# Optimization experiments

Measured on AMD Instinct MI355X. Metric: run time of the kernel, lower is better.

## Reference

```python
import jax, jax.numpy as jnp
import numpy as np

D_MODEL = 1024
NUM_HEADS = 16
HEAD_DIM = D_MODEL // NUM_HEADS


def setup_inputs() -> dict:
    key = jax.random.key(0)
    ks = jax.random.split(key, 11)
    B, S = 2, 2048
    scale = 1.0 / np.sqrt(D_MODEL)
    inp = {
        "query": jax.random.normal(ks[0], (B, S, D_MODEL), jnp.float32),
        "key": jax.random.normal(ks[1], (B, S, D_MODEL), jnp.float32),
        "value": jax.random.normal(ks[2], (B, S, D_MODEL), jnp.float32),
        "Wq": jax.random.normal(ks[3], (D_MODEL, D_MODEL), jnp.float32) * scale,
        "bq": jnp.zeros((D_MODEL,), jnp.float32),
        "Wk": jax.random.normal(ks[4], (D_MODEL, D_MODEL), jnp.float32) * scale,
        "bk": jnp.zeros((D_MODEL,), jnp.float32),
        "Wv": jax.random.normal(ks[5], (D_MODEL, D_MODEL), jnp.float32) * scale,
        "bv": jnp.zeros((D_MODEL,), jnp.float32),
        "Wo": jax.random.normal(ks[6], (D_MODEL, D_MODEL), jnp.float32) * scale,
        "bo": jnp.zeros((D_MODEL,), jnp.float32),
    }
    return inp


def _split_heads(x):
    # [B, S, D] -> [B, H, S, Dh]
    B, S, _ = x.shape
    return x.reshape(B, S, NUM_HEADS, HEAD_DIM).transpose(0, 2, 1, 3)


def reference(query, key, value, Wq, bq, Wk, bk, Wv, bv, Wo, bo):
    q = _split_heads(query @ Wq.T + bq)   # [B,H,S,Dh]
    k = _split_heads(key @ Wk.T + bk)
    v = _split_heads(value @ Wv.T + bv)
    scores = jnp.einsum('bhqd,bhkd->bhqk', q, k) / jnp.sqrt(
        jnp.asarray(HEAD_DIM, q.dtype))
    probs = jax.nn.softmax(scores, axis=-1)
    ctx = jnp.einsum('bhqk,bhkd->bhqd', probs, v)  # [B,H,S,Dh]
    B, H, S, Dh = ctx.shape
    ctx = ctx.transpose(0, 2, 1, 3).reshape(B, S, H * Dh)  # [B,S,D]
    return ctx @ Wo.T + bo
```

## Files before the change

### kernel.cpp

```cpp
#include <hip/hip_runtime.h>
#include <hip/hip_bf16.h>
#include <stdint.h>

#define D_MODEL 1024
#define NHEADS  16
#define HDIM    64
#define BATCH   2
#define SEQ     2048
#define MROWS   (BATCH*SEQ)

typedef __attribute__((ext_vector_type(8))) short  bf16x8;
typedef __attribute__((ext_vector_type(4))) float  f32x4;
typedef __attribute__((ext_vector_type(4))) int    int4v;

__device__ __forceinline__ unsigned short f2bf(float f) {
  unsigned int u = __float_as_uint(f);
  u = (u + 0x7fffu + ((u >> 16) & 1u)) >> 16;
  return (unsigned short)u;
}

__device__ __forceinline__ unsigned cvtpk_bf16(float lo, float hi) {
  unsigned r;
  asm("v_cvt_pk_bf16_f32 %0, %1, %2" : "=v"(r) : "v"(lo), "v"(hi));
  return r;
}

__device__ __forceinline__ int4v pack8(const float4& x, const float4& y) {
  int4v r;
  r[0] = (int)cvtpk_bf16(x.x, x.y);
  r[1] = (int)cvtpk_bf16(x.z, x.w);
  r[2] = (int)cvtpk_bf16(y.x, y.y);
  r[3] = (int)cvtpk_bf16(y.z, y.w);
  return r;
}

__device__ __forceinline__ void gload_lds16(const unsigned short* g, unsigned short* l) {
  __builtin_amdgcn_global_load_lds(
      (const __attribute__((address_space(1))) void*)g,
      (__attribute__((address_space(3))) void*)l,
      16, 0, 0);
}

__device__ __forceinline__ int swz_chunk(int row) { return (row + (row >> 3)) & 7; }
__device__ __forceinline__ int swz4(int row) { return (row + (row >> 2)) & 3; }
__device__ __forceinline__ int kperm(int m) {
  return (m & 0x63) | ((m & 0x10) >> 2) | ((m & 0x0C) << 1);
}

struct CvtArgs {
  const float* src[6];
  unsigned short* dst[6];
  int n[6];
};

__global__ __launch_bounds__(256) void cvt_all(CvtArgs a) {
  int t = blockIdx.y;
  const float* s = a.src[t];
  unsigned short* d = a.dst[t];
  int n = a.n[t];
  int stride = gridDim.x * blockDim.x * 4;
  for (int i = (blockIdx.x * blockDim.x + threadIdx.x) * 4; i < n; i += stride) {
    float4 v = *(const float4*)(s + i);
    ushort4 o;
    o.x = f2bf(v.x); o.y = f2bf(v.y); o.z = f2bf(v.z); o.w = f2bf(v.w);
    *(ushort4*)(d + i) = o;
  }
}

__device__ __forceinline__ void gemm_core(const unsigned short* __restrict__ X,
                                          const unsigned short* __restrict__ W,
                                          int m0, int n0,
                                          unsigned short* As, unsigned short* Bs,
                                          f32x4 (&acc)[4][4]) {
  const int tid  = threadIdx.x;
  const int lane = tid & 63;
  const int wv   = tid >> 6;
  const int wr   = wv >> 1, wc = wv & 1;
  const int srow = tid >> 3;
  const int scol = (((tid & 7) ^ (srow & 7)) * 8);
  const int sdst = tid * 16;

  for (int kt = 0; kt < D_MODEL / 64; ++kt) {
    __syncthreads();
    const unsigned short* Xs = X + (size_t)m0 * D_MODEL + kt * 64;
    const unsigned short* Ws = W + (size_t)n0 * D_MODEL + kt * 64;
#pragma unroll
    for (int c = 0; c < 4; ++c) {
      gload_lds16(Xs + (size_t)(srow + c * 32) * D_MODEL + scol,
                  (unsigned short*)((char*)As + sdst + c * 4096));
      gload_lds16(Ws + (size_t)(srow + c * 32) * D_MODEL + scol,
                  (unsigned short*)((char*)Bs + sdst + c * 4096));
    }
    __syncthreads();
#pragma unroll
    for (int kc = 0; kc < 2; ++kc) {
      bf16x8 af[4], bfv[4];
#pragma unroll
      for (int i = 0; i < 4; ++i) {
        int arow  = wr * 64 + i * 16 + (lane & 15);
        int abyte = (arow * 128 + (kc * 32 + 8 * (lane >> 4)) * 2) ^ ((arow & 7) << 4);
        af[i] = *(const bf16x8*)((const char*)As + abyte);
        int brow  = wc * 64 + i * 16 + (lane & 15);
        int bbyte = (brow * 128 + (kc * 32 + 8 * (lane >> 4)) * 2) ^ ((brow & 7) << 4);
        bfv[i] = *(const bf16x8*)((const char*)Bs + bbyte);
      }
#pragma unroll
      for (int mi = 0; mi < 4; ++mi)
#pragma unroll
        for (int ni = 0; ni < 4; ++ni)
          acc[mi][ni] = __builtin_amdgcn_mfma_f32_16x16x32_bf16(af[mi], bfv[ni],
                                                                acc[mi][ni], 0, 0, 0);
    }
  }
}

__global__ __launch_bounds__(256) void gemm_qkv(
    const unsigned short* __restrict__ Xq, const unsigned short* __restrict__ Xk,
    const unsigned short* __restrict__ Xv,
    const unsigned short* __restrict__ Wq, const unsigned short* __restrict__ Wk,
    const unsigned short* __restrict__ Wv,
    const float* __restrict__ bq, const float* __restrict__ bk,
    const float* __restrict__ bv,
    unsigned short* __restrict__ oq, unsigned short* __restrict__ ok,
    unsigned short* __restrict__ ov) {
  __shared__ __align__(16) unsigned short As[128 * 64];
  __shared__ __align__(16) unsigned short Bs[128 * 64];

  int fid   = blockIdx.x;
  int xcd   = fid & 7;
  int r_    = fid >> 3;
  int mloc  = r_ / 3;
  int nzloc = r_ % 3;
  int nz    = xcd * 3 + nzloc;
  int z     = nz >> 3;
  int n0    = (nz & 7) * 128;
  int m0    = mloc * 128;

  const unsigned short* X = (z == 0) ? Xq : (z == 1) ? Xk : Xv;
  const unsigned short* W = (z == 0) ? Wq : (z == 1) ? Wk : Wv;
  const float* bias       = (z == 0) ? bq : (z == 1) ? bk : bv;
  float scale = (z == 0) ? 0.18033688011112042f : 1.0f;

  f32x4 acc[4][4] = {};
  gemm_core(X, W, m0, n0, As, Bs, acc);

  const int lane = threadIdx.x & 63;
  const int wv   = threadIdx.x >> 6;
  const int wr   = wv >> 1, wc = wv & 1;
  const int g    = lane >> 4;
  const int cl   = lane & 15;

  if (z == 2) {
    int b = m0 >> 11;
    int sbase = (m0 & 2047) + wr * 64 + g * 4;
#pragma unroll
    for (int nj = 0; nj < 4; ++nj) {
      int n = n0 + wc * 64 + nj * 16 + cl;
      float bn = bias[n];
      unsigned short* vrow = ov + ((size_t)(b * 1024 + n)) * 2048;
#pragma unroll
      for (int mi = 0; mi < 4; ++mi) {
        int s = sbase + mi * 16;
        uint2 val;
        val.x = cvtpk_bf16(acc[mi][nj][0] + bn, acc[mi][nj][1] + bn);
        val.y = cvtpk_bf16(acc[mi][nj][2] + bn, acc[mi][nj][3] + bn);
        *(uint2*)(vrow + s) = val;
      }
    }
  } else {
    unsigned short* outp = (z == 0) ? oq : ok;
#pragma unroll
    for (int mi = 0; mi < 4; ++mi)
#pragma unroll
      for (int nj = 0; nj < 4; ++nj) {
        int n = n0 + wc * 64 + nj * 16 + cl;
        float bn = bias[n];
        int h = n >> 6, dh = n & 63;
#pragma unroll
        for (int rr = 0; rr < 4; ++rr) {
          int m = m0 + wr * 64 + mi * 16 + g * 4 + rr;
          float val = (acc[mi][nj][rr] + bn) * scale;
          int b = m >> 11, s = m & 2047;
          outp[(((size_t)(b * NHEADS + h)) * SEQ + s) * HDIM + dh] = f2bf(val);
        }
      }
  }
}

__global__ __launch_bounds__(512, 1) void gemm_out2(
    const unsigned short* __restrict__ Xc, const float* __restrict__ Wo,
    const float* __restrict__ bo, float* __restrict__ out) {
  __shared__ __align__(16) unsigned short LDS[2 * 8192];

  const int tid  = threadIdx.x;
  const int lane = tid & 63;
  const int w8   = tid >> 6;
  const int wr   = w8 >> 2;
  const int wc   = w8 & 3;
  const int g    = lane >> 4;
  const int cl   = lane & 15;

  int fid = blockIdx.x;
  int sid = (fid & 7) * 32 + (fid >> 3);
  int m0 = (sid >> 3) * 128;
  int n0 = (sid & 7) * 128;

  const int ar  = tid >> 2;
  const int as  = tid & 3;
  const int asw = swz4(ar);
  const unsigned short* Arow = Xc + (size_t)(m0 + ar) * D_MODEL + (as ^ asw) * 8;
  const float*          Brow = Wo + (size_t)(n0 + ar) * D_MODEL + (as ^ asw) * 8;
  const int bwb = ar * 64 + (as << 4);

  float4 rB0, rB1;
  auto gloadA = [&](int t, int bi) {
    gload_lds16(Arow + t * 32, LDS + bi * 8192 + tid * 8);
  };
  auto loadB = [&](int t) {
    const float* p = Brow + t * 32;
    rB0 = *(const float4*)(p);
    rB1 = *(const float4*)(p + 4);
  };
  auto writeB = [&](int bi) {
    char* B_ = (char*)(LDS + bi * 8192) + 8192;
    *(int4v*)(B_ + bwb) = pack8(rB0, rB1);
  };

  f32x4 acc[4][2] = {};

  gloadA(0, 0); loadB(0); writeB(0);
  __syncthreads();

#pragma unroll 2
  for (int t = 0; t < 32; ++t) {
    if (t < 31) { gloadA(t + 1, (t + 1) & 1); loadB(t + 1); }
    __builtin_amdgcn_sched_barrier(0);
    const char* Ab = (const char*)(LDS + (t & 1) * 8192);
    const char* Bb = Ab + 8192;
    bf16x8 af[4], bfr[2];
#pragma unroll
    for (int j = 0; j < 2; ++j) {
      int row = wc * 32 + j * 16 + cl;
      bfr[j] = *(const bf16x8*)(Bb + row * 64 + ((g ^ swz4(row)) << 4));
    }
#pragma unroll
    for (int i = 0; i < 4; ++i) {
      int row = wr * 64 + i * 16 + cl;
      af[i] = *(const bf16x8*)(Ab + row * 64 + ((g ^ swz4(row)) << 4));
    }
    __builtin_amdgcn_s_setprio(1);
#pragma unroll
    for (int i = 0; i < 4; ++i)
#pragma unroll
      for (int j = 0; j < 2; ++j)
        acc[i][j] = __builtin_amdgcn_mfma_f32_16x16x32_bf16(af[i], bfr[j],
                                                            acc[i][j], 0, 0, 0);
    __builtin_amdgcn_s_setprio(0);
    if (t < 31) writeB((t + 1) & 1);
    __syncthreads();
  }

#pragma unroll
  for (int mi = 0; mi < 4; ++mi)
#pragma unroll
    for (int nj = 0; nj < 2; ++nj) {
      int n = n0 + wc * 32 + nj * 16 + cl;
      float bn = bo[n];
#pragma unroll
      for (int rr = 0; rr < 4; ++rr) {
        int m = m0 + wr * 64 + mi * 16 + g * 4 + rr;
        out[(size_t)m * D_MODEL + n] = acc[mi][nj][rr] + bn;
      }
    }
}

__global__ __launch_bounds__(256, 2) void attn(
    const unsigned short* __restrict__ q, const unsigned short* __restrict__ k,
    const unsigned short* __restrict__ vt, unsigned short* __restrict__ ctx) {
  __shared__ __align__(16) unsigned short K0[128 * 64], V0[64 * 128];
  __shared__ __align__(16) unsigned short K1[128 * 64], V1[64 * 128];

  const int tid  = threadIdx.x;
  const int lane = tid & 63;
  const int wv   = tid >> 6;
  const int g    = lane >> 4;
  const int cl   = lane & 15;

  const int bh = blockIdx.x;
  const int qt = blockIdx.y;

  const unsigned short* qb  = q  + (size_t)bh * SEQ * HDIM;
  const unsigned short* kb  = k  + (size_t)bh * SEQ * HDIM;
  const unsigned short* vbt = vt + (size_t)bh * HDIM * SEQ;

  bf16x8 qf[2][2];
  {
    int qbase = qt * 128 + wv * 32;
#pragma unroll
    for (int qh = 0; qh < 2; ++qh) {
      const unsigned short* qp = qb + (size_t)(qbase + qh * 16 + cl) * HDIM + 8 * g;
      qf[qh][0] = *(const bf16x8*)(qp);
      qf[qh][1] = *(const bf16x8*)(qp + 32);
    }
  }

  const int srowK = tid >> 3;
  const int swzK  = swz_chunk(srowK);
  const int vrow  = tid >> 4;
  const int swzV  = swz_chunk(vrow);
  const int ldst  = tid * 16;

  f32x4 acc0[4] = {}, acc1[4] = {};
  f32x4 accs0 = {}, accs1 = {};
  const int4v onesi = {0x3F803F80, 0x3F803F80, 0x3F803F80, 0x3F803F80};
  const bf16x8 onesb = __builtin_bit_cast(bf16x8, onesi);

  auto stageK_ = [&](int t, unsigned short* Kb) {
    const unsigned short* kt_ = kb + (size_t)t * 128 * HDIM;
#pragma unroll
    for (int c = 0; c < 4; ++c) {
      int row  = srowK + 32 * c;
      int col  = ((tid & 7) ^ swzK ^ ((c & 1) << 2)) * 8;
      gload_lds16(kt_ + (size_t)kperm(row) * HDIM + col,
                  (unsigned short*)((char*)Kb + ldst + c * 4096));
    }
  };
  auto stageV_ = [&](int t, unsigned short* Vb) {
    const unsigned short* vt_ = vbt + t * 128;
#pragma unroll
    for (int c = 0; c < 4; ++c) {
      int row = vrow + 16 * c;
      int sw  = (swzV + 2 * c) & 7;
      int col = (((tid & 7) ^ sw) | (tid & 8)) * 8;
      gload_lds16(vt_ + (size_t)row * SEQ + col,
                  (unsigned short*)((char*)Vb + ldst + c * 4096));
    }
  };

  f32x4 sc[8][2];

  auto qk = [&](const unsigned short* Kb) {
#pragma unroll
    for (int ni = 0; ni < 8; ++ni) { sc[ni][0] = f32x4{}; sc[ni][1] = f32x4{}; }
    __builtin_amdgcn_s_setprio(1);
#pragma unroll
    for (int kc = 0; kc < 2; ++kc)
#pragma unroll
      for (int ni = 0; ni < 8; ++ni) {
        int row  = ni * 16 + cl;
        int byte = row * 128 + (((kc * 4 + g) ^ swz_chunk(row)) << 4);
        bf16x8 kf = *(const bf16x8*)((const char*)Kb + byte);
        sc[ni][0] = __builtin_amdgcn_mfma_f32_16x16x32_bf16(kf, qf[0][kc], sc[ni][0], 0, 0, 0);
        sc[ni][1] = __builtin_amdgcn_mfma_f32_16x16x32_bf16(kf, qf[1][kc], sc[ni][1], 0, 0, 0);
      }
    __builtin_amdgcn_s_setprio(0);
  };

  auto smpack = [&](int4v (&pa0)[4], int4v (&pa1)[4]) {
#pragma unroll
    for (int qh = 0; qh < 2; ++qh)
#pragma unroll
      for (int ni = 0; ni < 8; ++ni)
#pragma unroll
        for (int rr = 0; rr < 4; ++rr)
          sc[ni][qh][rr] = __builtin_amdgcn_exp2f(sc[ni][qh][rr]);
#pragma unroll
    for (int kcp = 0; kcp < 4; ++kcp) {
      pa0[kcp][0] = (int)cvtpk_bf16(sc[2 * kcp][0][0], sc[2 * kcp][0][1]);
      pa0[kcp][1] = (int)cvtpk_bf16(sc[2 * kcp][0][2], sc[2 * kcp][0][3]);
      pa0[kcp][2] = (int)cvtpk_bf16(sc[2 * kcp + 1][0][0], sc[2 * kcp + 1][0][1]);
      pa0[kcp][3] = (int)cvtpk_bf16(sc[2 * kcp + 1][0][2], sc[2 * kcp + 1][0][3]);
      pa1[kcp][0] = (int)cvtpk_bf16(sc[2 * kcp][1][0], sc[2 * kcp][1][1]);
      pa1[kcp][1] = (int)cvtpk_bf16(sc[2 * kcp][1][2], sc[2 * kcp][1][3]);
      pa1[kcp][2] = (int)cvtpk_bf16(sc[2 * kcp + 1][1][0], sc[2 * kcp + 1][1][1]);
      pa1[kcp][3] = (int)cvtpk_bf16(sc[2 * kcp + 1][1][2], sc[2 * kcp + 1][1][3]);
    }
  };

  auto pv = [&](const unsigned short* Vb, int4v (&pa0)[4], int4v (&pa1)[4]) {
    __builtin_amdgcn_s_setprio(1);
#pragma unroll
    for (int kcp = 0; kcp < 4; ++kcp) {
      bf16x8 a0 = __builtin_bit_cast(bf16x8, pa0[kcp]);
      bf16x8 a1 = __builtin_bit_cast(bf16x8, pa1[kcp]);
#pragma unroll
      for (int nd = 0; nd < 4; ++nd) {
        int row = nd * 16 + cl;
        int c   = kcp * 4 + g;
        int byte = row * 256 + ((((c & 7) ^ swz_chunk(row)) | (c & 8)) << 4);
        bf16x8 vf = *(const bf16x8*)((const char*)Vb + byte);
        acc0[nd] = __builtin_amdgcn_mfma_f32_16x16x32_bf16(a0, vf, acc0[nd], 0, 0, 0);
        acc1[nd] = __builtin_amdgcn_mfma_f32_16x16x32_bf16(a1, vf, acc1[nd], 0, 0, 0);
      }
      accs0 = __builtin_amdgcn_mfma_f32_16x16x32_bf16(a0, onesb, accs0, 0, 0, 0);
      accs1 = __builtin_amdgcn_mfma_f32_16x16x32_bf16(a1, onesb, accs1, 0, 0, 0);
    }
    __builtin_amdgcn_s_setprio(0);
  };

  const int NT = SEQ / 128;
  stageK_(0, K0);
  stageV_(0, V0);
  __syncthreads();
  stageK_(1, K1);
  qk(K0);
  for (int i = 0; i < NT; ++i) {
    int4v pa0[4], pa1[4];
    smpack(pa0, pa1);
    __syncthreads();
    if (i + 2 < NT) stageK_(i + 2, (i & 1) ? K1 : K0);
    if (i + 1 < NT) stageV_(i + 1, (i & 1) ? V0 : V1);
    if (i + 1 < NT) qk((i & 1) ? K0 : K1);
    pv((i & 1) ? V1 : V0, pa0, pa1);
  }

  int b = bh >> 4, h = bh & 15;
#pragma unroll
  for (int rr = 0; rr < 4; ++rr) {
    float i0 = 1.0f / accs0[rr];
    float i1 = 1.0f / accs1[rr];
#pragma unroll
    for (int qh = 0; qh < 2; ++qh) {
      int srow_o = qt * 128 + wv * 32 + qh * 16 + g * 4 + rr;
      float iv = qh ? i1 : i0;
#pragma unroll
      for (int nd = 0; nd < 4; ++nd) {
        int d = nd * 16 + cl;
        float val = (qh ? acc1[nd][rr] : acc0[nd][rr]) * iv;
        ctx[(((size_t)(b * SEQ + srow_o)) * NHEADS + h) * HDIM + d] = f2bf(val);
      }
    }
  }
}

extern "C" void kernel_launch(void* const* d_in, const int* in_sizes, int n_in,
                              void* d_out, int out_size, void* d_ws, size_t ws_size,
                              hipStream_t stream) {
  (void)in_sizes; (void)n_in; (void)out_size; (void)ws_size;
  const float* query = (const float*)d_in[0];
  const float* key_  = (const float*)d_in[1];
  const float* value = (const float*)d_in[2];
  const float* Wq = (const float*)d_in[3];
  const float* bq = (const float*)d_in[4];
  const float* Wk = (const float*)d_in[5];
  const float* bk = (const float*)d_in[6];
  const float* Wv = (const float*)d_in[7];
  const float* bv = (const float*)d_in[8];
  const float* Wo = (const float*)d_in[9];
  const float* bo = (const float*)d_in[10];
  float* out = (float*)d_out;

  unsigned short* w = (unsigned short*)d_ws;
  const size_t NA = (size_t)MROWS * D_MODEL;
  const size_t NW = (size_t)D_MODEL * D_MODEL;
  unsigned short* Xq  = w;
  unsigned short* Xk  = Xq + NA;
  unsigned short* Xv  = Xk + NA;
  unsigned short* Wqb = Xv + NA;
  unsigned short* Wkb = Wqb + NW;
  unsigned short* Wvb = Wkb + NW;
  unsigned short* qs  = Wvb + NW;
  unsigned short* ks  = qs + NA;
  unsigned short* vtb = ks + NA;
  unsigned short* cx  = vtb + NA;

  CvtArgs ca;
  ca.src[0] = query; ca.dst[0] = Xq;  ca.n[0] = (int)NA;
  ca.src[1] = key_;  ca.dst[1] = Xk;  ca.n[1] = (int)NA;
  ca.src[2] = value; ca.dst[2] = Xv;  ca.n[2] = (int)NA;
  ca.src[3] = Wq;    ca.dst[3] = Wqb; ca.n[3] = (int)NW;
  ca.src[4] = Wk;    ca.dst[4] = Wkb; ca.n[4] = (int)NW;
  ca.src[5] = Wv;    ca.dst[5] = Wvb; ca.n[5] = (int)NW;

  cvt_all<<<dim3(256, 6, 1), 256, 0, stream>>>(ca);
  gemm_qkv<<<dim3(768, 1, 1), 256, 0, stream>>>(Xq, Xk, Xv, Wqb, Wkb, Wvb,
                                                bq, bk, bv, qs, ks, vtb);
  attn<<<dim3(32, 16, 1), 256, 0, stream>>>(qs, ks, vtb, cx);
  gemm_out2<<<dim3(256, 1, 1), 512, 0, stream>>>(cx, Wo, bo, out);
}
```

Before: 126.9 us.

## Double per-wave query rows in attention to reuse K/V tiles across 64 rows

Each attention block now handles 256 query rows (64 per wave) instead of 128, so every staged K and V tile in shared memory feeds twice as many MFMAs. The grid is halved and launch bounds drop to one block per SIMD pair so the larger score and accumulator arrays fit in registers. The PV step is also moved ahead of the next QK inside the loop. The trade is fewer blocks (256) on the device and much higher register pressure, which lowers occupancy and may cause spills.

```diff
diff --git a/kernel.cpp b/kernel.cpp
--- a/kernel.cpp
+++ b/kernel.cpp
@@ -274,7 +274,7 @@
     }
 }
 
-__global__ __launch_bounds__(256, 2) void attn(
+__global__ __launch_bounds__(256, 1) void attn(
     const unsigned short* __restrict__ q, const unsigned short* __restrict__ k,
     const unsigned short* __restrict__ vt, unsigned short* __restrict__ ctx) {
   __shared__ __align__(16) unsigned short K0[128 * 64], V0[64 * 128];
@@ -293,11 +293,11 @@
   const unsigned short* kb  = k  + (size_t)bh * SEQ * HDIM;
   const unsigned short* vbt = vt + (size_t)bh * HDIM * SEQ;
 
-  bf16x8 qf[2][2];
+  bf16x8 qf[4][2];
   {
-    int qbase = qt * 128 + wv * 32;
-#pragma unroll
-    for (int qh = 0; qh < 2; ++qh) {
+    int qbase = qt * 256 + wv * 64;
+#pragma unroll
+    for (int qh = 0; qh < 4; ++qh) {
       const unsigned short* qp = qb + (size_t)(qbase + qh * 16 + cl) * HDIM + 8 * g;
       qf[qh][0] = *(const bf16x8*)(qp);
       qf[qh][1] = *(const bf16x8*)(qp + 32);
@@ -310,8 +310,8 @@
   const int swzV  = swz_chunk(vrow);
   const int ldst  = tid * 16;
 
-  f32x4 acc0[4] = {}, acc1[4] = {};
-  f32x4 accs0 = {}, accs1 = {};
+  f32x4 acc[4][4] = {};
+  f32x4 accs[4] = {};
   const int4v onesi = {0x3F803F80, 0x3F803F80, 0x3F803F80, 0x3F803F80};
   const bf16x8 onesb = __builtin_bit_cast(bf16x8, onesi);
 
@@ -337,11 +337,14 @@
     }
   };
 
-  f32x4 sc[8][2];
+  f32x4 sc[8][4];
+  int4v pa[4][4];
 
   auto qk = [&](const unsigned short* Kb) {
 #pragma unroll
-    for (int ni = 0; ni < 8; ++ni) { sc[ni][0] = f32x4{}; sc[ni][1] = f32x4{}; }
+    for (int ni = 0; ni < 8; ++ni)
+#pragma unroll
+      for (int qh = 0; qh < 4; ++qh) sc[ni][qh] = f32x4{};
     __builtin_amdgcn_s_setprio(1);
 #pragma unroll
     for (int kc = 0; kc < 2; ++kc)
@@ -350,50 +353,55 @@
         int row  = ni * 16 + cl;
         int byte = row * 128 + (((kc * 4 + g) ^ swz_chunk(row)) << 4);
         bf16x8 kf = *(const bf16x8*)((const char*)Kb + byte);
-        sc[ni][0] = __builtin_amdgcn_mfma_f32_16x16x32_bf16(kf, qf[0][kc], sc[ni][0], 0, 0, 0);
-        sc[ni][1] = __builtin_amdgcn_mfma_f32_16x16x32_bf16(kf, qf[1][kc], sc[ni][1], 0, 0, 0);
+#pragma unroll
+        for (int qh = 0; qh < 4; ++qh)
+          sc[ni][qh] = __builtin_amdgcn_mfma_f32_16x16x32_bf16(kf, qf[qh][kc],
+                                                               sc[ni][qh], 0, 0, 0);
       }
     __builtin_amdgcn_s_setprio(0);
   };
 
-  auto smpack = [&](int4v (&pa0)[4], int4v (&pa1)[4]) {
-#pragma unroll
-    for (int qh = 0; qh < 2; ++qh)
-#pragma unroll
-      for (int ni = 0; ni < 8; ++ni)
+  auto smpack = [&]() {
+#pragma unroll
+    for (int ni = 0; ni < 8; ++ni)
+#pragma unroll
+      for (int qh = 0; qh < 4; ++qh)
 #pragma unroll
         for (int rr = 0; rr < 4; ++rr)
           sc[ni][qh][rr] = __builtin_amdgcn_exp2f(sc[ni][qh][rr]);
 #pragma unroll
+    for (int kcp = 0; kcp < 4; ++kcp)
+#pragma unroll
+      for (int qh = 0; qh < 4; ++qh) {
+        pa[kcp][qh][0] = (int)cvtpk_bf16(sc[2 * kcp][qh][0], sc[2 * kcp][qh][1]);
+        pa[kcp][qh][1] = (int)cvtpk_bf16(sc[2 * kcp][qh][2], sc[2 * kcp][qh][3]);
+        pa[kcp][qh][2] = (int)cvtpk_bf16(sc[2 * kcp + 1][qh][0], sc[2 * kcp + 1][qh][1]);
+        pa[kcp][qh][3] = (int)cvtpk_bf16(sc[2 * kcp + 1][qh][2], sc[2 * kcp + 1][qh][3]);
+      }
+  };
+
+  auto pv = [&](const unsigned short* Vb) {
+    __builtin_amdgcn_s_setprio(1);
+#pragma unroll
     for (int kcp = 0; kcp < 4; ++kcp) {
-      pa0[kcp][0] = (int)cvtpk_bf16(sc[2 * kcp][0][0], sc[2 * kcp][0][1]);
-      pa0[kcp][1] = (int)cvtpk_bf16(sc[2 * kcp][0][2], sc[2 * kcp][0][3]);
-      pa0[kcp][2] = (int)cvtpk_bf16(sc[2 * kcp + 1][0][0], sc[2 * kcp + 1][0][1]);
-      pa0[kcp][3] = (int)cvtpk_bf16(sc[2 * kcp + 1][0][2], sc[2 * kcp + 1][0][3]);
-      pa1[kcp][0] = (int)cvtpk_bf16(sc[2 * kcp][1][0], sc[2 * kcp][1][1]);
-      pa1[kcp][1] = (int)cvtpk_bf16(sc[2 * kcp][1][2], sc[2 * kcp][1][3]);
-      pa1[kcp][2] = (int)cvtpk_bf16(sc[2 * kcp + 1][1][0], sc[2 * kcp + 1][1][1]);
-      pa1[kcp][3] = (int)cvtpk_bf16(sc[2 * kcp + 1][1][2], sc[2 * kcp + 1][1][3]);
-    }
-  };
-
-  auto pv = [&](const unsigned short* Vb, int4v (&pa0)[4], int4v (&pa1)[4]) {
-    __builtin_amdgcn_s_setprio(1);
-#pragma unroll
-    for (int kcp = 0; kcp < 4; ++kcp) {
-      bf16x8 a0 = __builtin_bit_cast(bf16x8, pa0[kcp]);
-      bf16x8 a1 = __builtin_bit_cast(bf16x8, pa1[kcp]);
 #pragma unroll
       for (int nd = 0; nd < 4; ++nd) {
         int row = nd * 16 + cl;
         int c   = kcp * 4 + g;
         int byte = row * 256 + ((((c & 7) ^ swz_chunk(row)) | (c & 8)) << 4);
         bf16x8 vf = *(const bf16x8*)((const char*)Vb + byte);
-        acc0[nd] = __builtin_amdgcn_mfma_f32_16x16x32_bf16(a0, vf, acc0[nd], 0, 0, 0);
-        acc1[nd] = __builtin_amdgcn_mfma_f32_16x16x32_bf16(a1, vf, acc1[nd], 0, 0, 0);
-      }
-      accs0 = __builtin_amdgcn_mfma_f32_16x16x32_bf16(a0, onesb, accs0, 0, 0, 0);
-      accs1 = __builtin_amdgcn_mfma_f32_16x16x32_bf16(a1, onesb, accs1, 0, 0, 0);
+#pragma unroll
+        for (int qh = 0; qh < 4; ++qh) {
+          bf16x8 a = __builtin_bit_cast(bf16x8, pa[kcp][qh]);
+          acc[nd][qh] = __builtin_amdgcn_mfma_f32_16x16x32_bf16(a, vf, acc[nd][qh],
+                                                                0, 0, 0);
+        }
+      }
+#pragma unroll
+      for (int qh = 0; qh < 4; ++qh) {
+        bf16x8 a = __builtin_bit_cast(bf16x8, pa[kcp][qh]);
+        accs[qh] = __builtin_amdgcn_mfma_f32_16x16x32_bf16(a, onesb, accs[qh], 0, 0, 0);
+      }
     }
     __builtin_amdgcn_s_setprio(0);
   };
@@ -405,32 +413,28 @@
   stageK_(1, K1);
   qk(K0);
   for (int i = 0; i < NT; ++i) {
-    int4v pa0[4], pa1[4];
-    smpack(pa0, pa1);
+    smpack();
     __syncthreads();
     if (i + 2 < NT) stageK_(i + 2, (i & 1) ? K1 : K0);
     if (i + 1 < NT) stageV_(i + 1, (i & 1) ? V0 : V1);
+    pv((i & 1) ? V1 : V0);
     if (i + 1 < NT) qk((i & 1) ? K0 : K1);
-    pv((i & 1) ? V1 : V0, pa0, pa1);
   }
 
   int b = bh >> 4, h = bh & 15;
 #pragma unroll
-  for (int rr = 0; rr < 4; ++rr) {
-    float i0 = 1.0f / accs0[rr];
-    float i1 = 1.0f / accs1[rr];
-#pragma unroll
-    for (int qh = 0; qh < 2; ++qh) {
-      int srow_o = qt * 128 + wv * 32 + qh * 16 + g * 4 + rr;
-      float iv = qh ? i1 : i0;
+  for (int qh = 0; qh < 4; ++qh)
+#pragma unroll
+    for (int rr = 0; rr < 4; ++rr) {
+      float iv = 1.0f / accs[qh][rr];
+      int srow_o = qt * 256 + wv * 64 + qh * 16 + g * 4 + rr;
 #pragma unroll
       for (int nd = 0; nd < 4; ++nd) {
         int d = nd * 16 + cl;
-        float val = (qh ? acc1[nd][rr] : acc0[nd][rr]) * iv;
-        ctx[(((size_t)(b * SEQ + srow_o)) * NHEADS + h) * HDIM + d] = f2bf(val);
-      }
-    }
-  }
+        ctx[(((size_t)(b * SEQ + srow_o)) * NHEADS + h) * HDIM + d] =
+            f2bf(acc[nd][qh][rr] * iv);
+      }
+    }
 }
 
 extern "C" void kernel_launch(void* const* d_in, const int* in_sizes, int n_in,
@@ -475,6 +479,6 @@
   cvt_all<<<dim3(256, 6, 1), 256, 0, stream>>>(ca);
   gemm_qkv<<<dim3(768, 1, 1), 256, 0, stream>>>(Xq, Xk, Xv, Wqb, Wkb, Wvb,
                                                 bq, bk, bv, qs, ks, vtb);
-  attn<<<dim3(32, 16, 1), 256, 0, stream>>>(qs, ks, vtb, cx);
+  attn<<<dim3(32, 8, 1), 256, 0, stream>>>(qs, ks, vtb, cx);
   gemm_out2<<<dim3(256, 1, 1), 512, 0, stream>>>(cx, Wo, bo, out);
 }
```

Measured after the change: 136.0 us. 7.2% more time.
